# Kernel tuning notes

Measured on AMD Instinct MI355X. Metric: run time of the kernel, lower is better.

## Reference

```python
import jax, jax.numpy as jnp
import numpy as np

MEMORY_COEF = 0.25
DHAT_COEF = 0.1

B, D, T, K = 64, 256, 512, 512
C, L = 8, 512


def setup_inputs() -> dict:
    key = jax.random.key(0)
    k1, k2, k3, k4, k5 = jax.random.split(key, 5)
    return {
        "Xhat": jax.random.normal(k1, (B, C, L), dtype=jnp.float32),
        "X": jax.random.normal(k2, (B, C, L), dtype=jnp.float32),
        "H": jax.random.normal(k3, (B, D, T), dtype=jnp.float32),
        "M": jax.random.normal(k4, (D, K), dtype=jnp.float32),
        "Dhat": jax.random.normal(k5, (B, T), dtype=jnp.float32),
    }


def _memory_loss(H, M):
    # H: [B, D, T]; M: [D, K] codebook with K codewords of dim D
    Ht = jnp.transpose(H, (0, 2, 1))  # [B, T, D]
    Mt = M.T                          # [K, D]
    # Squared distances via ||h||^2 - 2 h.m + ||m||^2 (argmin equals argmin of norms)
    d2 = (jnp.sum(Ht * Ht, axis=-1, keepdims=True)
          - 2.0 * jnp.einsum('btd,kd->btk', Ht, Mt)
          + jnp.sum(Mt * Mt, axis=-1))  # [B, T, K]
    idx = jnp.argmin(d2, axis=2)        # [B, T]
    Z = jnp.transpose(Mt[idx], (0, 2, 1))  # [B, D, T]
    sg = jax.lax.stop_gradient
    # ||.||^2 along dim D (norm then pow(2) == sum of squares)
    diffs = jnp.sum((sg(H) - Z) ** 2, axis=1) + jnp.sum((H - sg(Z)) ** 2, axis=1)  # [B, T]
    return jnp.sum(diffs) / float(np.prod(H.shape))


def reference(Xhat, X, H, M, Dhat):
    rec = jnp.mean((Xhat - X) ** 2)
    return rec + MEMORY_COEF * _memory_loss(H, M) - DHAT_COEF * jnp.mean(Dhat)
```

## Files before the change

### kernel.cpp

```cpp
#include <hip/hip_runtime.h>

#define NB   64
#define DD   256
#define TT   512
#define KK   512

typedef short bf8 __attribute__((ext_vector_type(8)));
typedef float f4  __attribute__((ext_vector_type(4)));

__device__ inline unsigned short f2bf(float x) {
  unsigned u = __float_as_uint(x);
  u += 0x7FFFu + ((u >> 16) & 1u);
  return (unsigned short)(u >> 16);
}

#define MFMA(accv, va, vb) \
  asm("v_mfma_f32_16x16x32_bf16 %0, %1, %2, %0" : "+v"(accv) : "v"(va), "v"(vb))

#define ACCROW(acc, kt) \
    "+v"(acc[kt][0]), "+v"(acc[kt][1]), "+v"(acc[kt][2]), "+v"(acc[kt][3]), \
    "+v"(acc[kt][4]), "+v"(acc[kt][5]), "+v"(acc[kt][6]), "+v"(acc[kt][7])
#define ACCLIST8(acc) ACCROW(acc,0), ACCROW(acc,1), ACCROW(acc,2), ACCROW(acc,3)

__global__ __launch_bounds__(256) void edm_prep(
    const float* __restrict__ M, const float4* __restrict__ Xh,
    const float4* __restrict__ X, const float4* __restrict__ Dh,
    unsigned short* __restrict__ Mt, float* __restrict__ mnorm,
    float* __restrict__ recp, float* __restrict__ dhp) {
  __shared__ __align__(16) float tile[DD][68];
  __shared__ float pn[4][64];
  __shared__ float ps[8];

  const int bid  = blockIdx.x;
  const int tid  = threadIdx.x;
  const int lane = tid & 63;
  const int q    = tid >> 6;

  if (bid < 8) {
    #pragma unroll
    for (int it = 0; it < 16; ++it) {
      const int d  = q * 64 + it * 4 + (lane >> 4);
      const int kc = (lane & 15) << 2;
      const float4 v = *(const float4*)(M + (size_t)d * KK + bid * 64 + kc);
      *(float4*)&tile[d][kc] = v;
    }
    __syncthreads();
    const int k = bid * 64 + lane;
    float s = 0.f;
    #pragma unroll
    for (int c = 0; c < 8; ++c) {
      unsigned pk[4];
      #pragma unroll
      for (int e = 0; e < 4; ++e) {
        const float x0 = tile[q * 64 + c * 8 + 2 * e + 0][lane];
        const float x1 = tile[q * 64 + c * 8 + 2 * e + 1][lane];
        s += x0 * x0 + x1 * x1;
        pk[e] = (unsigned)f2bf(x0) | ((unsigned)f2bf(x1) << 16);
      }
      *(uint4*)(Mt + (size_t)k * DD + q * 64 + c * 8) =
          make_uint4(pk[0], pk[1], pk[2], pk[3]);
    }
    pn[q][lane] = s;
    __syncthreads();
    if (q == 0) mnorm[k] = pn[0][lane] + pn[1][lane] + pn[2][lane] + pn[3][lane];
  } else {
    const int r = bid - 8;
    float s = 0.f, sd = 0.f;
    #pragma unroll
    for (int i = 0; i < 4; ++i) {
      const int idx = r * 1024 + i * 256 + tid;
      const float4 a = Xh[idx];
      const float4 c = X[idx];
      const float e0 = a.x - c.x, e1 = a.y - c.y, e2 = a.z - c.z, e3 = a.w - c.w;
      s += e0 * e0 + e1 * e1 + e2 * e2 + e3 * e3;
    }
    if (tid < 128) {
      const float4 dd = Dh[r * 128 + tid];
      sd = dd.x + dd.y + dd.z + dd.w;
    }
    #pragma unroll
    for (int off = 32; off > 0; off >>= 1) {
      s  += __shfl_down(s, off);
      sd += __shfl_down(sd, off);
    }
    if (lane == 0) { ps[q] = s; ps[4 + q] = sd; }
    __syncthreads();
    if (tid == 0) {
      recp[r] = ps[0] + ps[1] + ps[2] + ps[3];
      dhp[r]  = ps[4] + ps[5] + ps[6] + ps[7];
    }
  }
}

__global__ __launch_bounds__(512, 2) void edm_main(
    const float* __restrict__ H, const unsigned short* __restrict__ Mt,
    const float* __restrict__ mnorm, float* __restrict__ d2part) {
  __shared__ __align__(16) float scratch[64][132];
  __shared__ __align__(16) unsigned short Hbf[128 * 256];
  __shared__ float hsum[128];
  __shared__ float wmin[8][128];
  __shared__ float bsum[2];

  const int tid = threadIdx.x;
  const int b   = blockIdx.x >> 2;
  const int t0  = (blockIdx.x & 3) << 7;
  const float* Hb = H + (size_t)b * DD * TT + t0;

  if (tid < 128) hsum[tid] = 0.f;

  const int tcol = tid & 127;
  const int q    = tid >> 7;
  float hacc = 0.f;

  for (int ch = 0; ch < 4; ++ch) {
    #pragma unroll
    for (int ii = 0; ii < 4; ++ii) {
      const int f  = ii * 512 + tid;
      const int dl = f >> 5;
      const int t4 = (f & 31) << 2;
      const float4 v = *(const float4*)(Hb + (size_t)(ch * 64 + dl) * TT + t4);
      *(float4*)&scratch[dl][t4] = v;
    }
    __syncthreads();
    unsigned wpk[8];
    #pragma unroll
    for (int jj = 0; jj < 8; ++jj) {
      const float x0 = scratch[q * 16 + 2 * jj + 0][tcol];
      const float x1 = scratch[q * 16 + 2 * jj + 1][tcol];
      hacc += x0 * x0 + x1 * x1;
      wpk[jj] = (unsigned)f2bf(x0) | ((unsigned)f2bf(x1) << 16);
    }
    char* rowp = (char*)Hbf + tcol * 512;
    const int dbase2 = (ch * 64 + q * 16) * 2;
    const int swz = (tcol & 7) << 4;
    *(uint4*)(rowp + ((dbase2 +  0) ^ swz)) = make_uint4(wpk[0], wpk[1], wpk[2], wpk[3]);
    *(uint4*)(rowp + ((dbase2 + 16) ^ swz)) = make_uint4(wpk[4], wpk[5], wpk[6], wpk[7]);
    __syncthreads();
  }
  atomicAdd(&hsum[tcol], hacc);

  const int l   = tid & 63;
  const int wv  = tid >> 6;
  const int kb  = wv << 6;
  const int r16 = l & 15;
  const int g   = l >> 4;

  float rmin[8] = {3.0e38f, 3.0e38f, 3.0e38f, 3.0e38f,
                   3.0e38f, 3.0e38f, 3.0e38f, 3.0e38f};
  f4 acc[4][8];
  #pragma unroll
  for (int kt = 0; kt < 4; ++kt)
    #pragma unroll
    for (int tn = 0; tn < 8; ++tn)
      acc[kt][tn] = (f4){0.f, 0.f, 0.f, 0.f};
  asm volatile("s_nop 1" : ACCLIST8(acc));

  #pragma unroll
  for (int ds = 0; ds < 8; ++ds) {
    bf8 afr[4];
    #pragma unroll
    for (int kt = 0; kt < 4; ++kt)
      afr[kt] = *(const bf8*)(Mt + (size_t)(kb + kt * 16 + r16) * DD + ds * 32 + g * 8);
    #pragma unroll
    for (int tn = 0; tn < 8; ++tn) {
      const int t = tn * 16 + r16;
      const bf8 bfr = *(const bf8*)((const char*)Hbf + t * 512 +
                                    ((ds * 64 + g * 16) ^ ((t & 7) << 4)));
      MFMA(acc[0][tn], afr[0], bfr);
      MFMA(acc[1][tn], afr[1], bfr);
      MFMA(acc[2][tn], afr[2], bfr);
      MFMA(acc[3][tn], afr[3], bfr);
    }
  }
  asm volatile("s_nop 7\n\ts_nop 7" : ACCLIST8(acc));

  #pragma unroll
  for (int kt = 0; kt < 4; ++kt) {
    const f4 mn = *(const f4*)(mnorm + kb + kt * 16 + g * 4);
    #pragma unroll
    for (int tn = 0; tn < 8; ++tn) {
      #pragma unroll
      for (int rr = 0; rr < 4; ++rr) {
        const float d2 = mn[rr] - 2.f * acc[kt][tn][rr];
        rmin[tn] = fminf(rmin[tn], d2);
      }
    }
  }

  #pragma unroll
  for (int tn = 0; tn < 8; ++tn) {
    rmin[tn] = fminf(rmin[tn], __shfl_xor(rmin[tn], 16));
    rmin[tn] = fminf(rmin[tn], __shfl_xor(rmin[tn], 32));
  }
  if (g == 0) {
    #pragma unroll
    for (int tn = 0; tn < 8; ++tn) wmin[wv][tn * 16 + r16] = rmin[tn];
  }
  __syncthreads();

  if (tid < 128) {
    float m = wmin[0][tid];
    #pragma unroll
    for (int w = 1; w < 8; ++w) m = fminf(m, wmin[w][tid]);
    float v = m + hsum[tid];
    #pragma unroll
    for (int off = 32; off > 0; off >>= 1) v += __shfl_down(v, off);
    if ((tid & 63) == 0) bsum[tid >> 6] = v;
  }
  __syncthreads();
  if (tid == 0) d2part[blockIdx.x] = bsum[0] + bsum[1];
}

__global__ __launch_bounds__(256) void edm_fin(
    const float* __restrict__ recp, const float* __restrict__ dhp,
    const float* __restrict__ d2p, float* __restrict__ out) {
  const int tid = threadIdx.x;
  float a  = d2p[tid];
  float r  = (tid < 64) ? recp[tid] : 0.f;
  float dh = (tid < 64) ? dhp[tid]  : 0.f;
  #pragma unroll
  for (int off = 32; off > 0; off >>= 1) {
    a  += __shfl_down(a, off);
    r  += __shfl_down(r, off);
    dh += __shfl_down(dh, off);
  }
  __shared__ float pa[4], pr[4], pd[4];
  const int w = tid >> 6;
  if ((tid & 63) == 0) { pa[w] = a; pr[w] = r; pd[w] = dh; }
  __syncthreads();
  if (tid == 0) {
    const float d2sum  = pa[0] + pa[1] + pa[2] + pa[3];
    const float recsum = pr[0] + pr[1] + pr[2] + pr[3];
    const float dhsum  = pd[0] + pd[1] + pd[2] + pd[3];
    out[0] = recsum * (1.f / 262144.f)
           + d2sum  * (1.f / 16777216.f)
           - 0.1f * dhsum * (1.f / 32768.f);
  }
}

extern "C" void kernel_launch(void* const* d_in, const int* in_sizes, int n_in,
                              void* d_out, int out_size, void* d_ws, size_t ws_size,
                              hipStream_t stream) {
  const float* Xh = (const float*)d_in[0];
  const float* X  = (const float*)d_in[1];
  const float* H  = (const float*)d_in[2];
  const float* M  = (const float*)d_in[3];
  const float* Dh = (const float*)d_in[4];
  float* out = (float*)d_out;

  unsigned short* Mt = (unsigned short*)d_ws;
  float* mnorm = (float*)((char*)d_ws + (size_t)KK * DD * 2);
  float* recp  = mnorm + KK;
  float* dhp   = recp + 64;
  float* d2p   = dhp + 64;

  edm_prep<<<72, 256, 0, stream>>>(M, (const float4*)Xh, (const float4*)X,
                                   (const float4*)Dh, Mt, mnorm, recp, dhp);
  edm_main<<<NB * (TT / 128), 512, 0, stream>>>(H, Mt, mnorm, d2p);
  edm_fin<<<1, 256, 0, stream>>>(recp, dhp, d2p, out);
}
```

Measured before the change: 26.49 us.

## Switch to 32x32 MFMA with fragment-ordered codebook, smaller tiles, fused final reduction

The codebook is repacked in the prep kernel into an MFMA-fragment order, so each lane loads its A fragment contiguously. The main kernel switches from 16x16x32 to 32x32x16 bf16 MFMA and halves the per-block tile to 64 timesteps with 256 threads, giving 512 blocks. The separate final kernel is removed: the last block, detected through an atomic counter reset in the prep kernel, performs the global reduction. This aims to cut launch overhead, improve MFMA efficiency and raise parallelism, at the cost of atomic/fence ordering complexity and more codebook reloads across blocks.

```diff
diff --git a/kernel.cpp b/kernel.cpp
--- a/kernel.cpp
+++ b/kernel.cpp
@@ -5,28 +5,29 @@
 #define TT   512
 #define KK   512
 
-typedef short bf8 __attribute__((ext_vector_type(8)));
-typedef float f4  __attribute__((ext_vector_type(4)));
-
-__device__ inline unsigned short f2bf(float x) {
+typedef short bf8  __attribute__((ext_vector_type(8)));
+typedef float f4   __attribute__((ext_vector_type(4)));
+typedef float f16v __attribute__((ext_vector_type(16)));
+
+__device__ inline unsigned f2bf(float x) {
   unsigned u = __float_as_uint(x);
   u += 0x7FFFu + ((u >> 16) & 1u);
-  return (unsigned short)(u >> 16);
-}
-
-#define MFMA(accv, va, vb) \
-  asm("v_mfma_f32_16x16x32_bf16 %0, %1, %2, %0" : "+v"(accv) : "v"(va), "v"(vb))
-
-#define ACCROW(acc, kt) \
-    "+v"(acc[kt][0]), "+v"(acc[kt][1]), "+v"(acc[kt][2]), "+v"(acc[kt][3]), \
-    "+v"(acc[kt][4]), "+v"(acc[kt][5]), "+v"(acc[kt][6]), "+v"(acc[kt][7])
-#define ACCLIST8(acc) ACCROW(acc,0), ACCROW(acc,1), ACCROW(acc,2), ACCROW(acc,3)
+  return u >> 16;
+}
+
+#define MFMA32(accv, va, vb) \
+  asm("v_mfma_f32_32x32x16_bf16 %0, %1, %2, %0" : "+v"(accv) : "v"(va), "v"(vb))
+
+#define ACC8(acc) \
+  "+v"(acc[0][0]), "+v"(acc[0][1]), "+v"(acc[1][0]), "+v"(acc[1][1]), \
+  "+v"(acc[2][0]), "+v"(acc[2][1]), "+v"(acc[3][0]), "+v"(acc[3][1])
 
 __global__ __launch_bounds__(256) void edm_prep(
     const float* __restrict__ M, const float4* __restrict__ Xh,
     const float4* __restrict__ X, const float4* __restrict__ Dh,
-    unsigned short* __restrict__ Mt, float* __restrict__ mnorm,
-    float* __restrict__ recp, float* __restrict__ dhp) {
+    unsigned short* __restrict__ MtF, float* __restrict__ mnorm,
+    float* __restrict__ recp, float* __restrict__ dhp,
+    unsigned* __restrict__ counter) {
   __shared__ __align__(16) float tile[DD][68];
   __shared__ float pn[4][64];
   __shared__ float ps[8];
@@ -36,29 +37,36 @@
   const int lane = tid & 63;
   const int q    = tid >> 6;
 
+  if (bid == 0 && tid == 0) *counter = 0u;
+
   if (bid < 8) {
     #pragma unroll
     for (int it = 0; it < 16; ++it) {
       const int d  = q * 64 + it * 4 + (lane >> 4);
       const int kc = (lane & 15) << 2;
-      const float4 v = *(const float4*)(M + (size_t)d * KK + bid * 64 + kc);
-      *(float4*)&tile[d][kc] = v;
-    }
-    __syncthreads();
-    const int k = bid * 64 + lane;
+      *(float4*)&tile[d][kc] = *(const float4*)(M + (size_t)d * KK + bid * 64 + kc);
+    }
+    __syncthreads();
+    const int k   = bid * 64 + lane;
+    const int K32 = k >> 5;
+    const int c   = k & 31;
     float s = 0.f;
     #pragma unroll
-    for (int c = 0; c < 8; ++c) {
-      unsigned pk[4];
+    for (int dsl = 0; dsl < 4; ++dsl) {
+      const int ds = q * 4 + dsl;
       #pragma unroll
-      for (int e = 0; e < 4; ++e) {
-        const float x0 = tile[q * 64 + c * 8 + 2 * e + 0][lane];
-        const float x1 = tile[q * 64 + c * 8 + 2 * e + 1][lane];
-        s += x0 * x0 + x1 * x1;
-        pk[e] = (unsigned)f2bf(x0) | ((unsigned)f2bf(x1) << 16);
+      for (int h = 0; h < 2; ++h) {
+        unsigned pk[4];
+        #pragma unroll
+        for (int e = 0; e < 4; ++e) {
+          const float x0 = tile[ds * 16 + h * 8 + 2 * e + 0][lane];
+          const float x1 = tile[ds * 16 + h * 8 + 2 * e + 1][lane];
+          s += x0 * x0 + x1 * x1;
+          pk[e] = f2bf(x0) | (f2bf(x1) << 16);
+        }
+        *(uint4*)(MtF + ((size_t)(K32 * 16 + ds) * 64 + c + 32 * h) * 8) =
+            make_uint4(pk[0], pk[1], pk[2], pk[3]);
       }
-      *(uint4*)(Mt + (size_t)k * DD + q * 64 + c * 8) =
-          make_uint4(pk[0], pk[1], pk[2], pk[3]);
     }
     pn[q][lane] = s;
     __syncthreads();
@@ -92,34 +100,37 @@
   }
 }
 
-__global__ __launch_bounds__(512, 2) void edm_main(
-    const float* __restrict__ H, const unsigned short* __restrict__ Mt,
-    const float* __restrict__ mnorm, float* __restrict__ d2part) {
-  __shared__ __align__(16) float scratch[64][132];
-  __shared__ __align__(16) unsigned short Hbf[128 * 256];
-  __shared__ float hsum[128];
-  __shared__ float wmin[8][128];
-  __shared__ float bsum[2];
+__global__ __launch_bounds__(256, 2) void edm_main(
+    const float* __restrict__ H, const unsigned short* __restrict__ MtF,
+    const float* __restrict__ mnorm, const float* __restrict__ recp,
+    const float* __restrict__ dhp, float* __restrict__ d2part,
+    unsigned* __restrict__ counter, float* __restrict__ out) {
+  __shared__ __align__(16) float scratch[64][68];
+  __shared__ __align__(16) unsigned short Hbf[64 * 256];
+  __shared__ float hsum[64];
+  __shared__ float wmin[4][64];
+  __shared__ float red[12];
+  __shared__ int   islast;
 
   const int tid = threadIdx.x;
-  const int b   = blockIdx.x >> 2;
-  const int t0  = (blockIdx.x & 3) << 7;
+  const int b   = blockIdx.x >> 3;
+  const int t0  = (blockIdx.x & 7) << 6;
   const float* Hb = H + (size_t)b * DD * TT + t0;
 
-  if (tid < 128) hsum[tid] = 0.f;
-
-  const int tcol = tid & 127;
-  const int q    = tid >> 7;
+  if (tid < 64) hsum[tid] = 0.f;
+
+  const int tcol = tid & 63;
+  const int q    = tid >> 6;
   float hacc = 0.f;
 
   for (int ch = 0; ch < 4; ++ch) {
     #pragma unroll
     for (int ii = 0; ii < 4; ++ii) {
-      const int f  = ii * 512 + tid;
-      const int dl = f >> 5;
-      const int t4 = (f & 31) << 2;
-      const float4 v = *(const float4*)(Hb + (size_t)(ch * 64 + dl) * TT + t4);
-      *(float4*)&scratch[dl][t4] = v;
+      const int f  = ii * 256 + tid;
+      const int dl = f >> 4;
+      const int t4 = (f & 15) << 2;
+      *(float4*)&scratch[dl][t4] =
+          *(const float4*)(Hb + (size_t)(ch * 64 + dl) * TT + t4);
     }
     __syncthreads();
     unsigned wpk[8];
@@ -128,7 +139,7 @@
       const float x0 = scratch[q * 16 + 2 * jj + 0][tcol];
       const float x1 = scratch[q * 16 + 2 * jj + 1][tcol];
       hacc += x0 * x0 + x1 * x1;
-      wpk[jj] = (unsigned)f2bf(x0) | ((unsigned)f2bf(x1) << 16);
+      wpk[jj] = f2bf(x0) | (f2bf(x1) << 16);
     }
     char* rowp = (char*)Hbf + tcol * 512;
     const int dbase2 = (ch * 64 + q * 16) * 2;
@@ -139,102 +150,98 @@
   }
   atomicAdd(&hsum[tcol], hacc);
 
-  const int l   = tid & 63;
-  const int wv  = tid >> 6;
-  const int kb  = wv << 6;
-  const int r16 = l & 15;
-  const int g   = l >> 4;
-
-  float rmin[8] = {3.0e38f, 3.0e38f, 3.0e38f, 3.0e38f,
-                   3.0e38f, 3.0e38f, 3.0e38f, 3.0e38f};
-  f4 acc[4][8];
+  const int l  = tid & 63;
+  const int wv = tid >> 6;
+  const int kb = wv << 7;
+  const int h  = l >> 5;
+  const int c  = l & 31;
+
+  f16v acc[4][2];
   #pragma unroll
   for (int kt = 0; kt < 4; ++kt)
     #pragma unroll
-    for (int tn = 0; tn < 8; ++tn)
-      acc[kt][tn] = (f4){0.f, 0.f, 0.f, 0.f};
-  asm volatile("s_nop 1" : ACCLIST8(acc));
-
-  #pragma unroll
-  for (int ds = 0; ds < 8; ++ds) {
+    for (int tn = 0; tn < 2; ++tn)
+      #pragma unroll
+      for (int r = 0; r < 16; ++r) acc[kt][tn][r] = 0.f;
+  asm volatile("s_nop 1" : ACC8(acc));
+
+  #pragma unroll 2
+  for (int ds = 0; ds < 16; ++ds) {
     bf8 afr[4];
     #pragma unroll
     for (int kt = 0; kt < 4; ++kt)
-      afr[kt] = *(const bf8*)(Mt + (size_t)(kb + kt * 16 + r16) * DD + ds * 32 + g * 8);
-    #pragma unroll
-    for (int tn = 0; tn < 8; ++tn) {
-      const int t = tn * 16 + r16;
+      afr[kt] = *(const bf8*)(MtF + ((size_t)((wv * 4 + kt) * 16 + ds) * 64 + l) * 8);
+    #pragma unroll
+    for (int tn = 0; tn < 2; ++tn) {
+      const int t = tn * 32 + c;
       const bf8 bfr = *(const bf8*)((const char*)Hbf + t * 512 +
-                                    ((ds * 64 + g * 16) ^ ((t & 7) << 4)));
-      MFMA(acc[0][tn], afr[0], bfr);
-      MFMA(acc[1][tn], afr[1], bfr);
-      MFMA(acc[2][tn], afr[2], bfr);
-      MFMA(acc[3][tn], afr[3], bfr);
-    }
-  }
-  asm volatile("s_nop 7\n\ts_nop 7" : ACCLIST8(acc));
-
+                                    ((ds * 32 + h * 16) ^ ((t & 7) << 4)));
+      MFMA32(acc[0][tn], afr[0], bfr);
+      MFMA32(acc[1][tn], afr[1], bfr);
+      MFMA32(acc[2][tn], afr[2], bfr);
+      MFMA32(acc[3][tn], afr[3], bfr);
+    }
+  }
+  asm volatile("s_nop 7\n\ts_nop 7\n\ts_nop 7" : ACC8(acc));
+
+  float rmin[2] = {3.0e38f, 3.0e38f};
   #pragma unroll
   for (int kt = 0; kt < 4; ++kt) {
-    const f4 mn = *(const f4*)(mnorm + kb + kt * 16 + g * 4);
-    #pragma unroll
-    for (int tn = 0; tn < 8; ++tn) {
+    #pragma unroll
+    for (int seg = 0; seg < 4; ++seg) {
+      const f4 mn = *(const f4*)(mnorm + kb + kt * 32 + seg * 8 + h * 4);
       #pragma unroll
       for (int rr = 0; rr < 4; ++rr) {
-        const float d2 = mn[rr] - 2.f * acc[kt][tn][rr];
-        rmin[tn] = fminf(rmin[tn], d2);
+        const int r = seg * 4 + rr;
+        rmin[0] = fminf(rmin[0], mn[rr] - 2.f * acc[kt][0][r]);
+        rmin[1] = fminf(rmin[1], mn[rr] - 2.f * acc[kt][1][r]);
       }
     }
   }
-
-  #pragma unroll
-  for (int tn = 0; tn < 8; ++tn) {
-    rmin[tn] = fminf(rmin[tn], __shfl_xor(rmin[tn], 16));
-    rmin[tn] = fminf(rmin[tn], __shfl_xor(rmin[tn], 32));
-  }
-  if (g == 0) {
-    #pragma unroll
-    for (int tn = 0; tn < 8; ++tn) wmin[wv][tn * 16 + r16] = rmin[tn];
-  }
+  rmin[0] = fminf(rmin[0], __shfl_xor(rmin[0], 32));
+  rmin[1] = fminf(rmin[1], __shfl_xor(rmin[1], 32));
+  if (h == 0) { wmin[wv][c] = rmin[0]; wmin[wv][32 + c] = rmin[1]; }
   __syncthreads();
 
-  if (tid < 128) {
-    float m = wmin[0][tid];
-    #pragma unroll
-    for (int w = 1; w < 8; ++w) m = fminf(m, wmin[w][tid]);
-    float v = m + hsum[tid];
+  if (tid < 64) {
+    float v = fminf(fminf(wmin[0][tid], wmin[1][tid]),
+                    fminf(wmin[2][tid], wmin[3][tid])) + hsum[tid];
     #pragma unroll
     for (int off = 32; off > 0; off >>= 1) v += __shfl_down(v, off);
-    if ((tid & 63) == 0) bsum[tid >> 6] = v;
+    if (tid == 0)
+      __hip_atomic_store(&d2part[blockIdx.x], v, __ATOMIC_RELEASE,
+                         __HIP_MEMORY_SCOPE_AGENT);
+  }
+
+  if (tid == 0) {
+    __threadfence();
+    islast = (atomicAdd(counter, 1u) == 511u) ? 1 : 0;
   }
   __syncthreads();
-  if (tid == 0) d2part[blockIdx.x] = bsum[0] + bsum[1];
-}
-
-__global__ __launch_bounds__(256) void edm_fin(
-    const float* __restrict__ recp, const float* __restrict__ dhp,
-    const float* __restrict__ d2p, float* __restrict__ out) {
-  const int tid = threadIdx.x;
-  float a  = d2p[tid];
-  float r  = (tid < 64) ? recp[tid] : 0.f;
-  float dh = (tid < 64) ? dhp[tid]  : 0.f;
-  #pragma unroll
-  for (int off = 32; off > 0; off >>= 1) {
-    a  += __shfl_down(a, off);
-    r  += __shfl_down(r, off);
-    dh += __shfl_down(dh, off);
-  }
-  __shared__ float pa[4], pr[4], pd[4];
-  const int w = tid >> 6;
-  if ((tid & 63) == 0) { pa[w] = a; pr[w] = r; pd[w] = dh; }
-  __syncthreads();
-  if (tid == 0) {
-    const float d2sum  = pa[0] + pa[1] + pa[2] + pa[3];
-    const float recsum = pr[0] + pr[1] + pr[2] + pr[3];
-    const float dhsum  = pd[0] + pd[1] + pd[2] + pd[3];
-    out[0] = recsum * (1.f / 262144.f)
-           + d2sum  * (1.f / 16777216.f)
-           - 0.1f * dhsum * (1.f / 32768.f);
+  if (islast) {
+    float a = __hip_atomic_load(&d2part[tid], __ATOMIC_RELAXED,
+                                __HIP_MEMORY_SCOPE_AGENT)
+            + __hip_atomic_load(&d2part[tid + 256], __ATOMIC_RELAXED,
+                                __HIP_MEMORY_SCOPE_AGENT);
+    float r  = (tid < 64) ? recp[tid] : 0.f;
+    float dh = (tid < 64) ? dhp[tid]  : 0.f;
+    #pragma unroll
+    for (int off = 32; off > 0; off >>= 1) {
+      a  += __shfl_down(a, off);
+      r  += __shfl_down(r, off);
+      dh += __shfl_down(dh, off);
+    }
+    const int w = tid >> 6;
+    if ((tid & 63) == 0) { red[w] = a; red[4 + w] = r; red[8 + w] = dh; }
+    __syncthreads();
+    if (tid == 0) {
+      const float d2sum  = red[0] + red[1] + red[2] + red[3];
+      const float recsum = red[4] + red[5] + red[6] + red[7];
+      const float dhsum  = red[8] + red[9] + red[10] + red[11];
+      out[0] = recsum * (1.f / 262144.f)
+             + d2sum  * (1.f / 16777216.f)
+             - 0.1f * dhsum * (1.f / 32768.f);
+    }
   }
 }
 
@@ -248,14 +255,16 @@
   const float* Dh = (const float*)d_in[4];
   float* out = (float*)d_out;
 
-  unsigned short* Mt = (unsigned short*)d_ws;
+  unsigned short* MtF = (unsigned short*)d_ws;
   float* mnorm = (float*)((char*)d_ws + (size_t)KK * DD * 2);
   float* recp  = mnorm + KK;
   float* dhp   = recp + 64;
   float* d2p   = dhp + 64;
+  unsigned* counter = (unsigned*)(d2p + 512);
 
   edm_prep<<<72, 256, 0, stream>>>(M, (const float4*)Xh, (const float4*)X,
-                                   (const float4*)Dh, Mt, mnorm, recp, dhp);
-  edm_main<<<NB * (TT / 128), 512, 0, stream>>>(H, Mt, mnorm, d2p);
-  edm_fin<<<1, 256, 0, stream>>>(recp, dhp, d2p, out);
-}
+                                   (const float4*)Dh, MtF, mnorm, recp, dhp,
+                                   counter);
+  edm_main<<<NB * (TT / 64), 256, 0, stream>>>(H, MtF, mnorm, recp, dhp,
+                                               d2p, counter, out);
+}
```

After: 35.21 us. 1.33x slower.

## Pipeline H loads via LDS DMA, fragment-order codebook, fuse final reduction

Applied to the files above, without the earlier changes.

H chunks now stream into a double-buffered LDS scratch through global_load_lds DMA. Each chunk's bf16 conversion overlaps with the next chunk's load and with MFMA work on the previous one. The codebook is written in MFMA fragment order so each A-fragment is one coalesced 16-byte load, and those loads are issued early per chunk. The separate final kernel is replaced by a last-block-done atomic counter, which saves a launch but adds release/acquire atomics and hand-tuned waitcnt ordering that could be fragile.

```diff
diff --git a/kernel.cpp b/kernel.cpp
--- a/kernel.cpp
+++ b/kernel.cpp
@@ -8,10 +8,10 @@
 typedef short bf8 __attribute__((ext_vector_type(8)));
 typedef float f4  __attribute__((ext_vector_type(4)));
 
-__device__ inline unsigned short f2bf(float x) {
+__device__ inline unsigned f2bf(float x) {
   unsigned u = __float_as_uint(x);
   u += 0x7FFFu + ((u >> 16) & 1u);
-  return (unsigned short)(u >> 16);
+  return u >> 16;
 }
 
 #define MFMA(accv, va, vb) \
@@ -22,11 +22,21 @@
     "+v"(acc[kt][4]), "+v"(acc[kt][5]), "+v"(acc[kt][6]), "+v"(acc[kt][7])
 #define ACCLIST8(acc) ACCROW(acc,0), ACCROW(acc,1), ACCROW(acc,2), ACCROW(acc,3)
 
+#define GLOAD16(dst, src) \
+  asm volatile("global_load_dwordx4 %0, %1, off" : "=v"(dst) : "v"(src))
+
+__device__ inline void gload_lds16(const void* g, void* l) {
+  __builtin_amdgcn_global_load_lds(
+      (const __attribute__((address_space(1))) unsigned*)g,
+      (__attribute__((address_space(3))) unsigned*)l, 16, 0, 0);
+}
+
 __global__ __launch_bounds__(256) void edm_prep(
     const float* __restrict__ M, const float4* __restrict__ Xh,
     const float4* __restrict__ X, const float4* __restrict__ Dh,
-    unsigned short* __restrict__ Mt, float* __restrict__ mnorm,
-    float* __restrict__ recp, float* __restrict__ dhp) {
+    unsigned short* __restrict__ MtF, float* __restrict__ mnorm,
+    float* __restrict__ recp, float* __restrict__ dhp,
+    unsigned* __restrict__ counter) {
   __shared__ __align__(16) float tile[DD][68];
   __shared__ float pn[4][64];
   __shared__ float ps[8];
@@ -36,29 +46,36 @@
   const int lane = tid & 63;
   const int q    = tid >> 6;
 
+  if (bid == 0 && tid == 0) *counter = 0u;
+
   if (bid < 8) {
     #pragma unroll
     for (int it = 0; it < 16; ++it) {
       const int d  = q * 64 + it * 4 + (lane >> 4);
       const int kc = (lane & 15) << 2;
-      const float4 v = *(const float4*)(M + (size_t)d * KK + bid * 64 + kc);
-      *(float4*)&tile[d][kc] = v;
+      *(float4*)&tile[d][kc] = *(const float4*)(M + (size_t)d * KK + bid * 64 + kc);
     }
     __syncthreads();
-    const int k = bid * 64 + lane;
+    const int k    = bid * 64 + lane;
+    const int k16  = k >> 4;
+    const int r16k = k & 15;
     float s = 0.f;
     #pragma unroll
-    for (int c = 0; c < 8; ++c) {
-      unsigned pk[4];
-      #pragma unroll
-      for (int e = 0; e < 4; ++e) {
-        const float x0 = tile[q * 64 + c * 8 + 2 * e + 0][lane];
-        const float x1 = tile[q * 64 + c * 8 + 2 * e + 1][lane];
-        s += x0 * x0 + x1 * x1;
-        pk[e] = (unsigned)f2bf(x0) | ((unsigned)f2bf(x1) << 16);
+    for (int dsl = 0; dsl < 2; ++dsl) {
+      const int ds = q * 2 + dsl;
+      #pragma unroll
+      for (int g = 0; g < 4; ++g) {
+        unsigned pk[4];
+        #pragma unroll
+        for (int e = 0; e < 4; ++e) {
+          const float x0 = tile[ds * 32 + g * 8 + 2 * e + 0][lane];
+          const float x1 = tile[ds * 32 + g * 8 + 2 * e + 1][lane];
+          s += x0 * x0 + x1 * x1;
+          pk[e] = f2bf(x0) | (f2bf(x1) << 16);
+        }
+        *(uint4*)(MtF + ((size_t)(k16 * 8 + ds) * 64 + r16k + 16 * g) * 8) =
+            make_uint4(pk[0], pk[1], pk[2], pk[3]);
       }
-      *(uint4*)(Mt + (size_t)k * DD + q * 64 + c * 8) =
-          make_uint4(pk[0], pk[1], pk[2], pk[3]);
     }
     pn[q][lane] = s;
     __syncthreads();
@@ -93,60 +110,32 @@
 }
 
 __global__ __launch_bounds__(512, 2) void edm_main(
-    const float* __restrict__ H, const unsigned short* __restrict__ Mt,
-    const float* __restrict__ mnorm, float* __restrict__ d2part) {
-  __shared__ __align__(16) float scratch[64][132];
+    const float* __restrict__ H, const unsigned short* __restrict__ MtF,
+    const float* __restrict__ mnorm, const float* __restrict__ recp,
+    const float* __restrict__ dhp, float* __restrict__ d2part,
+    unsigned* __restrict__ counter, float* __restrict__ out) {
+  __shared__ __align__(16) float scratch[2][64][128];
   __shared__ __align__(16) unsigned short Hbf[128 * 256];
   __shared__ float hsum[128];
   __shared__ float wmin[8][128];
+  __shared__ float red[12];
   __shared__ float bsum[2];
-
-  const int tid = threadIdx.x;
-  const int b   = blockIdx.x >> 2;
-  const int t0  = (blockIdx.x & 3) << 7;
-  const float* Hb = H + (size_t)b * DD * TT + t0;
-
-  if (tid < 128) hsum[tid] = 0.f;
-
+  __shared__ int   islast;
+
+  const int tid  = threadIdx.x;
+  const int wv   = tid >> 6;
+  const int l    = tid & 63;
   const int tcol = tid & 127;
   const int q    = tid >> 7;
-  float hacc = 0.f;
-
-  for (int ch = 0; ch < 4; ++ch) {
-    #pragma unroll
-    for (int ii = 0; ii < 4; ++ii) {
-      const int f  = ii * 512 + tid;
-      const int dl = f >> 5;
-      const int t4 = (f & 31) << 2;
-      const float4 v = *(const float4*)(Hb + (size_t)(ch * 64 + dl) * TT + t4);
-      *(float4*)&scratch[dl][t4] = v;
-    }
-    __syncthreads();
-    unsigned wpk[8];
-    #pragma unroll
-    for (int jj = 0; jj < 8; ++jj) {
-      const float x0 = scratch[q * 16 + 2 * jj + 0][tcol];
-      const float x1 = scratch[q * 16 + 2 * jj + 1][tcol];
-      hacc += x0 * x0 + x1 * x1;
-      wpk[jj] = (unsigned)f2bf(x0) | ((unsigned)f2bf(x1) << 16);
-    }
-    char* rowp = (char*)Hbf + tcol * 512;
-    const int dbase2 = (ch * 64 + q * 16) * 2;
-    const int swz = (tcol & 7) << 4;
-    *(uint4*)(rowp + ((dbase2 +  0) ^ swz)) = make_uint4(wpk[0], wpk[1], wpk[2], wpk[3]);
-    *(uint4*)(rowp + ((dbase2 + 16) ^ swz)) = make_uint4(wpk[4], wpk[5], wpk[6], wpk[7]);
-    __syncthreads();
-  }
-  atomicAdd(&hsum[tcol], hacc);
-
-  const int l   = tid & 63;
-  const int wv  = tid >> 6;
-  const int kb  = wv << 6;
-  const int r16 = l & 15;
-  const int g   = l >> 4;
-
-  float rmin[8] = {3.0e38f, 3.0e38f, 3.0e38f, 3.0e38f,
-                   3.0e38f, 3.0e38f, 3.0e38f, 3.0e38f};
+  const int r16  = l & 15;
+  const int g    = l >> 4;
+
+  const int b  = blockIdx.x >> 2;
+  const int t0 = (blockIdx.x & 3) << 7;
+  const float* Hb = H + (size_t)b * DD * TT + t0;
+
+  if (tid < 128) hsum[tid] = 0.f;
+
   f4 acc[4][8];
   #pragma unroll
   for (int kt = 0; kt < 4; ++kt)
@@ -155,38 +144,93 @@
       acc[kt][tn] = (f4){0.f, 0.f, 0.f, 0.f};
   asm volatile("s_nop 1" : ACCLIST8(acc));
 
+  #define ISSUE_DMA(buf, ch)                                                  \
+    {                                                                         \
+      _Pragma("unroll")                                                       \
+      for (int ii = 0; ii < 4; ++ii) {                                        \
+        const int f  = ii * 512 + wv * 64;             \
+        const int fl = f + l;                                                 \
+        const int dl = fl >> 5;                                               \
+        const int t4 = (fl & 31) << 2;                                        \
+        gload_lds16(Hb + (size_t)((ch) * 64 + dl) * TT + t4,                  \
+                    (char*)&scratch[buf][0][0] + (size_t)f * 16);             \
+      }                                                                       \
+    }
+
+  ISSUE_DMA(0, 0);
+  float hacc = 0.f;
+
   #pragma unroll
-  for (int ds = 0; ds < 8; ++ds) {
-    bf8 afr[4];
-    #pragma unroll
-    for (int kt = 0; kt < 4; ++kt)
-      afr[kt] = *(const bf8*)(Mt + (size_t)(kb + kt * 16 + r16) * DD + ds * 32 + g * 8);
-    #pragma unroll
-    for (int tn = 0; tn < 8; ++tn) {
-      const int t = tn * 16 + r16;
-      const bf8 bfr = *(const bf8*)((const char*)Hbf + t * 512 +
-                                    ((ds * 64 + g * 16) ^ ((t & 7) << 4)));
-      MFMA(acc[0][tn], afr[0], bfr);
-      MFMA(acc[1][tn], afr[1], bfr);
-      MFMA(acc[2][tn], afr[2], bfr);
-      MFMA(acc[3][tn], afr[3], bfr);
+  for (int ch = 0; ch < 4; ++ch) {
+    bf8 afr[2][4];
+    #pragma unroll
+    for (int s = 0; s < 2; ++s)
+      #pragma unroll
+      for (int kt = 0; kt < 4; ++kt)
+        GLOAD16(afr[s][kt],
+                (const void*)((const char*)MtF +
+                              (((size_t)(wv * 4 + kt) * 8 + ch * 2 + s) * 64 + l) * 16));
+    __builtin_amdgcn_sched_barrier(0);
+    if (ch < 3) ISSUE_DMA((ch + 1) & 1, ch + 1);
+    __builtin_amdgcn_sched_barrier(0);
+    if (ch < 3) asm volatile("s_waitcnt vmcnt(12)" ::: "memory");
+    else        asm volatile("s_waitcnt vmcnt(8)"  ::: "memory");
+    __builtin_amdgcn_s_barrier();
+    asm volatile("" ::: "memory");
+
+    {
+      unsigned wpk[8];
+      #pragma unroll
+      for (int jj = 0; jj < 8; ++jj) {
+        const float x0 = scratch[ch & 1][q * 16 + 2 * jj + 0][tcol];
+        const float x1 = scratch[ch & 1][q * 16 + 2 * jj + 1][tcol];
+        hacc += x0 * x0 + x1 * x1;
+        wpk[jj] = f2bf(x0) | (f2bf(x1) << 16);
+      }
+      char* rowp = (char*)Hbf + tcol * 512;
+      const int dbase2 = (ch * 64 + q * 16) * 2;
+      const int swz = (tcol & 7) << 4;
+      *(uint4*)(rowp + ((dbase2 +  0) ^ swz)) = make_uint4(wpk[0], wpk[1], wpk[2], wpk[3]);
+      *(uint4*)(rowp + ((dbase2 + 16) ^ swz)) = make_uint4(wpk[4], wpk[5], wpk[6], wpk[7]);
+    }
+    asm volatile("s_waitcnt lgkmcnt(0)" ::: "memory");
+    __builtin_amdgcn_s_barrier();
+    asm volatile("" ::: "memory");
+    if (ch < 3) asm volatile("s_waitcnt vmcnt(4)" ::: "memory");
+    else        asm volatile("s_waitcnt vmcnt(0)" ::: "memory");
+    __builtin_amdgcn_sched_barrier(0);
+
+    #pragma unroll
+    for (int s = 0; s < 2; ++s) {
+      const int ds = ch * 2 + s;
+      #pragma unroll
+      for (int tn = 0; tn < 8; ++tn) {
+        const int t = tn * 16 + r16;
+        const bf8 bfr = *(const bf8*)((const char*)Hbf + t * 512 +
+                                      ((ds * 64 + g * 16) ^ ((t & 7) << 4)));
+        MFMA(acc[0][tn], afr[s][0], bfr);
+        MFMA(acc[1][tn], afr[s][1], bfr);
+        MFMA(acc[2][tn], afr[s][2], bfr);
+        MFMA(acc[3][tn], afr[s][3], bfr);
+      }
     }
   }
   asm volatile("s_nop 7\n\ts_nop 7" : ACCLIST8(acc));
 
+  atomicAdd(&hsum[tcol], hacc);
+
+  float rmin[8] = {3.0e38f, 3.0e38f, 3.0e38f, 3.0e38f,
+                   3.0e38f, 3.0e38f, 3.0e38f, 3.0e38f};
   #pragma unroll
   for (int kt = 0; kt < 4; ++kt) {
-    const f4 mn = *(const f4*)(mnorm + kb + kt * 16 + g * 4);
+    const f4 mn = *(const f4*)(mnorm + wv * 64 + kt * 16 + g * 4);
     #pragma unroll
     for (int tn = 0; tn < 8; ++tn) {
       #pragma unroll
-      for (int rr = 0; rr < 4; ++rr) {
-        const float d2 = mn[rr] - 2.f * acc[kt][tn][rr];
-        rmin[tn] = fminf(rmin[tn], d2);
-      }
-    }
-  }
-
+      for (int rr = 0; rr < 4; ++rr)
+        rmin[tn] = fminf(rmin[tn], mn[rr] - 2.f * acc[kt][tn][rr]);
+    }
+  }
   #pragma unroll
   for (int tn = 0; tn < 8; ++tn) {
     rmin[tn] = fminf(rmin[tn], __shfl_xor(rmin[tn], 16));
@@ -208,33 +252,40 @@
     if ((tid & 63) == 0) bsum[tid >> 6] = v;
   }
   __syncthreads();
-  if (tid == 0) d2part[blockIdx.x] = bsum[0] + bsum[1];
-}
-
-__global__ __launch_bounds__(256) void edm_fin(
-    const float* __restrict__ recp, const float* __restrict__ dhp,
-    const float* __restrict__ d2p, float* __restrict__ out) {
-  const int tid = threadIdx.x;
-  float a  = d2p[tid];
-  float r  = (tid < 64) ? recp[tid] : 0.f;
-  float dh = (tid < 64) ? dhp[tid]  : 0.f;
-  #pragma unroll
-  for (int off = 32; off > 0; off >>= 1) {
-    a  += __shfl_down(a, off);
-    r  += __shfl_down(r, off);
-    dh += __shfl_down(dh, off);
-  }
-  __shared__ float pa[4], pr[4], pd[4];
-  const int w = tid >> 6;
-  if ((tid & 63) == 0) { pa[w] = a; pr[w] = r; pd[w] = dh; }
+  if (tid == 0) {
+    __hip_atomic_store(&d2part[blockIdx.x], bsum[0] + bsum[1],
+                       __ATOMIC_RELEASE, __HIP_MEMORY_SCOPE_AGENT);
+    islast = (__hip_atomic_fetch_add(counter, 1u, __ATOMIC_ACQ_REL,
+                                     __HIP_MEMORY_SCOPE_AGENT) == 255u) ? 1 : 0;
+  }
   __syncthreads();
-  if (tid == 0) {
-    const float d2sum  = pa[0] + pa[1] + pa[2] + pa[3];
-    const float recsum = pr[0] + pr[1] + pr[2] + pr[3];
-    const float dhsum  = pd[0] + pd[1] + pd[2] + pd[3];
-    out[0] = recsum * (1.f / 262144.f)
-           + d2sum  * (1.f / 16777216.f)
-           - 0.1f * dhsum * (1.f / 32768.f);
+
+  if (islast) {
+    float a = 0.f, r = 0.f, dh = 0.f;
+    if (tid < 256) {
+      a = __hip_atomic_load(&d2part[tid], __ATOMIC_RELAXED,
+                            __HIP_MEMORY_SCOPE_AGENT);
+      if (tid < 64) { r = recp[tid]; dh = dhp[tid]; }
+    }
+    #pragma unroll
+    for (int off = 32; off > 0; off >>= 1) {
+      a  += __shfl_down(a, off);
+      r  += __shfl_down(r, off);
+      dh += __shfl_down(dh, off);
+    }
+    if (tid < 256 && (tid & 63) == 0) {
+      const int w = tid >> 6;
+      red[w] = a; red[4 + w] = r; red[8 + w] = dh;
+    }
+    __syncthreads();
+    if (tid == 0) {
+      const float d2sum  = red[0] + red[1] + red[2] + red[3];
+      const float recsum = red[4] + red[5] + red[6] + red[7];
+      const float dhsum  = red[8] + red[9] + red[10] + red[11];
+      out[0] = recsum * (1.f / 262144.f)
+             + d2sum  * (1.f / 16777216.f)
+             - 0.1f * dhsum * (1.f / 32768.f);
+    }
   }
 }
 
@@ -248,14 +299,16 @@
   const float* Dh = (const float*)d_in[4];
   float* out = (float*)d_out;
 
-  unsigned short* Mt = (unsigned short*)d_ws;
+  unsigned short* MtF = (unsigned short*)d_ws;
   float* mnorm = (float*)((char*)d_ws + (size_t)KK * DD * 2);
   float* recp  = mnorm + KK;
   float* dhp   = recp + 64;
   float* d2p   = dhp + 64;
+  unsigned* counter = (unsigned*)(d2p + 256);
 
   edm_prep<<<72, 256, 0, stream>>>(M, (const float4*)Xh, (const float4*)X,
-                                   (const float4*)Dh, Mt, mnorm, recp, dhp);
-  edm_main<<<NB * (TT / 128), 512, 0, stream>>>(H, Mt, mnorm, d2p);
-  edm_fin<<<1, 256, 0, stream>>>(recp, dhp, d2p, out);
-}
+                                   (const float4*)Dh, MtF, mnorm, recp, dhp,
+                                   counter);
+  edm_main<<<NB * (TT / 128), 512, 0, stream>>>(H, MtF, mnorm, recp, dhp,
+                                                d2p, counter, out);
+}
```

New measurement: 29.50 us. 1.11x slower.
